# Kernel optimization log

Hardware: AMD Instinct MI355X
Metric: run time of the kernel (lower is better)

Reference implementation:

```python
import jax, jax.numpy as jnp
import numpy as np

N, IN_F, OUT_F, H = 8192, 256, 64, 4
NEG_SLOPE = 0.2


def setup_inputs() -> dict:
    key = jax.random.key(0)
    ks = jax.random.split(key, 8)
    inputs = jax.random.normal(ks[0], (N, IN_F), dtype=jnp.float32)
    # sparse-ish binary adjacency with self loops (sparse.softmax only sees nonzeros)
    adj = (jax.random.uniform(ks[1], (N, N)) < 0.05).astype(jnp.float32)
    idx = jnp.arange(N)
    adj = adj.at[idx, idx].set(1.0)
    stdv = 1.0 / np.sqrt(H * OUT_F)
    weight = jax.random.uniform(ks[2], (IN_F, H * OUT_F), minval=-stdv, maxval=stdv, dtype=jnp.float32)
    bias = jax.random.uniform(ks[3], (1, H * OUT_F), minval=-stdv, maxval=stdv, dtype=jnp.float32)
    # weight_u/v: stdv = 1/sqrt(size(-1)=1) = 1
    weight_u = jax.random.uniform(ks[4], (H, OUT_F, 1), minval=-1.0, maxval=1.0, dtype=jnp.float32)
    weight_v = jax.random.uniform(ks[5], (H, OUT_F, 1), minval=-1.0, maxval=1.0, dtype=jnp.float32)
    stdp = 1.0 / np.sqrt(IN_F)
    proj_w = jax.random.uniform(ks[6], (H * OUT_F, IN_F), minval=-stdp, maxval=stdp, dtype=jnp.float32)
    proj_b = jax.random.uniform(ks[7], (H * OUT_F,), minval=-stdp, maxval=stdp, dtype=jnp.float32)
    return {"inputs": inputs, "adj_mat": adj, "weight": weight, "weight_u": weight_u,
            "weight_v": weight_v, "bias": bias, "proj_w": proj_w, "proj_b": proj_b}


def reference(inputs, adj_mat, weight, weight_u, weight_v, bias, proj_w, proj_b):
    n = inputs.shape[0]
    support = (inputs @ weight).reshape(n, H, OUT_F).transpose(1, 0, 2)  # [H,N,O]
    f1 = jnp.einsum('hno,ho->hn', support, weight_u[..., 0])  # [H,N]
    f2 = jnp.einsum('hno,ho->hn', support, weight_v[..., 0])  # [H,N]
    logits = f1[:, None, :] + f2[:, :, None]                  # [H,N,N]
    w = jax.nn.leaky_relu(logits, NEG_SLOPE)
    masked = w * adj_mat                                      # adj broadcast over heads
    mask = adj_mat != 0.0
    # sparse.softmax over dim 2: softmax restricted to nonzero (edge) positions
    neg = jnp.where(mask, masked, -jnp.inf)
    m = jnp.max(neg, axis=2, keepdims=True)
    m = jnp.where(jnp.isfinite(m), m, 0.0)
    e = jnp.where(mask, jnp.exp(neg - m), 0.0)
    denom = jnp.sum(e, axis=2, keepdims=True)
    attn = e / jnp.where(denom > 0, denom, 1.0)               # [H,N,N]
    out = jnp.einsum('hnm,hmo->hno', attn, support)           # [H,N,O]
    out = out.transpose(1, 0, 2).reshape(n, H * OUT_F)
    out = out + bias
    out = out + inputs @ proj_w.T + proj_b
    return out
```

## Files before the change

kernel.cpp:

```cpp
#include <hip/hip_runtime.h>
#include <hip/hip_bf16.h>

#define N_NODES 8192
#define IN_FEAT 256
#define OUT_F   64
#define NHEAD   4
#define HF      256
#define NEG     0.2f

typedef unsigned short u16;
typedef unsigned long long u64;
typedef __attribute__((ext_vector_type(8))) short short8;
typedef __attribute__((ext_vector_type(4))) float f32x4;

__device__ __forceinline__ u16 f2bf(float f) {
    union { unsigned int u; float f; } v; v.f = f;
    unsigned int r = v.u + 0x7FFFu + ((v.u >> 16) & 1u);
    return (u16)(r >> 16);
}

__global__ __launch_bounds__(256) void k_tr(const float* __restrict__ PW,
                                            float* __restrict__ PWT) {
    __shared__ float t[64][65];
    const int bx = (blockIdx.x & 3) * 64;
    const int by = (blockIdx.x >> 2) * 64;
    const int tx = threadIdx.x & 63;
    const int ty = threadIdx.x >> 6;
    #pragma unroll
    for (int r = ty; r < 64; r += 4)
        t[r][tx] = PW[(size_t)(by + r) * IN_FEAT + bx + tx];
    __syncthreads();
    #pragma unroll
    for (int r = ty; r < 64; r += 4)
        PWT[(size_t)(bx + r) * HF + by + tx] = t[tx][r];
}

#define RPB 4
__global__ __launch_bounds__(256, 8) void k_gemm(
    const float* __restrict__ inp,
    const float* __restrict__ W,
    const float* __restrict__ U,
    const float* __restrict__ V,
    const float* __restrict__ Bias,
    const float* __restrict__ PWT,
    const float* __restrict__ PB,
    const float* __restrict__ adj,
    u16*   __restrict__ suppB,
    float* __restrict__ f1,
    float* __restrict__ f2,
    float* __restrict__ outp,
    u16*   __restrict__ gb,
    float* __restrict__ anum,
    float* __restrict__ aden)
{
    __shared__ __align__(16) float in_lds[RPB][IN_FEAT];
    const int c  = threadIdx.x;
    const int n0 = blockIdx.x * RPB;

    #pragma unroll
    for (int r = 0; r < RPB; ++r)
        in_lds[r][c] = inp[(size_t)(n0 + r) * IN_FEAT + c];
    __syncthreads();

    float accs[RPB], accp[RPB];
    #pragma unroll
    for (int r = 0; r < RPB; ++r) { accs[r] = 0.f; accp[r] = 0.f; }

    const float* wc = W   + c;
    const float* pc = PWT + c;
    float w0 = wc[0 * HF], w1 = wc[1 * HF], w2 = wc[2 * HF], w3 = wc[3 * HF];
    float p0 = pc[0 * HF], p1 = pc[1 * HF], p2 = pc[2 * HF], p3 = pc[3 * HF];

    #pragma unroll 1
    for (int k = 0; k < IN_FEAT; k += 4) {
        const int kn = (k + 4) & 255;
        const float nw0 = wc[(kn + 0) * HF];
        const float nw1 = wc[(kn + 1) * HF];
        const float nw2 = wc[(kn + 2) * HF];
        const float nw3 = wc[(kn + 3) * HF];
        const float np0 = pc[(kn + 0) * HF];
        const float np1 = pc[(kn + 1) * HF];
        const float np2 = pc[(kn + 2) * HF];
        const float np3 = pc[(kn + 3) * HF];
        #pragma unroll
        for (int r = 0; r < RPB; ++r) {
            const float4 xv = *(const float4*)&in_lds[r][k];
            accs[r] = fmaf(xv.x, w0, accs[r]);
            accs[r] = fmaf(xv.y, w1, accs[r]);
            accs[r] = fmaf(xv.z, w2, accs[r]);
            accs[r] = fmaf(xv.w, w3, accs[r]);
            accp[r] = fmaf(xv.x, p0, accp[r]);
            accp[r] = fmaf(xv.y, p1, accp[r]);
            accp[r] = fmaf(xv.z, p2, accp[r]);
            accp[r] = fmaf(xv.w, p3, accp[r]);
        }
        w0 = nw0; w1 = nw1; w2 = nw2; w3 = nw3;
        p0 = np0; p1 = np1; p2 = np2; p3 = np3;
    }

    const int h = c >> 6, lane = c & 63;
    const float uv = U[c], vv = V[c];
    const float bb = Bias[c] + PB[c];

    {
        const int o   = c & 63;
        const int t   = o >> 4;
        const int cc  = o & 15;
        const int jbg = n0 >> 5;
        const int q   = (n0 & 31) >> 3;
        const int el  = n0 & 7;
        union { short s[4]; u64 q8; } sv;
        #pragma unroll
        for (int r = 0; r < RPB; ++r) sv.s[r] = (short)f2bf(accs[r]);
        const size_t word = ((size_t)(h * 256 + jbg) * 4 + t) * 64 + (q << 4) + cc;
        *(u64*)(suppB + word * 8 + el) = sv.q8;
    }

    #pragma unroll
    for (int r = 0; r < RPB; ++r) {
        float s1 = accs[r] * uv, s2 = accs[r] * vv;
        #pragma unroll
        for (int mm = 32; mm > 0; mm >>= 1) {
            s1 += __shfl_xor(s1, mm);
            s2 += __shfl_xor(s2, mm);
        }
        if (lane == 0) {
            f1[h * N_NODES + n0 + r] = s1;
            f2[h * N_NODES + n0 + r] = s2;
        }
        outp[(size_t)(n0 + r) * HF + c] = accp[r] + bb;
    }

    #pragma unroll
    for (int r = 0; r < RPB; ++r)
        anum[(size_t)(n0 + r) * HF + c] = 0.f;
    if (c < 16)
        aden[(size_t)(c >> 2) * N_NODES + n0 + (c & 3)] = 0.f;

    #pragma unroll
    for (int r = 0; r < RPB; ++r) {
        const float* ar = adj + (size_t)(n0 + r) * N_NODES;
        u16* gr = gb + (size_t)(n0 + r) * 1024;
        #pragma unroll
        for (int pass = 0; pass < 4; ++pass) {
            const int w = pass * 256 + c;
            const float4 a0 = *(const float4*)(ar + w * 8);
            const float4 a1 = *(const float4*)(ar + w * 8 + 4);
            gr[w] = (u16)(
                (unsigned)(a0.x != 0.f)        | ((unsigned)(a0.y != 0.f) << 1) |
                ((unsigned)(a0.z != 0.f) << 2) | ((unsigned)(a0.w != 0.f) << 3) |
                ((unsigned)(a1.x != 0.f) << 8) | ((unsigned)(a1.y != 0.f) << 9) |
                ((unsigned)(a1.z != 0.f) << 10)| ((unsigned)(a1.w != 0.f) << 11));
        }
    }
}

__global__ __launch_bounds__(256) void k_prep(const float* __restrict__ f1,
                                              float* __restrict__ f1max,
                                              float* __restrict__ EAB) {
    __shared__ float red[256];
    const int h = blockIdx.x;
    float m = -1e30f;
    for (int j = threadIdx.x; j < N_NODES; j += 256)
        m = fmaxf(m, f1[h * N_NODES + j]);
    red[threadIdx.x] = m;
    __syncthreads();
    for (int s = 128; s > 0; s >>= 1) {
        if (threadIdx.x < s) red[threadIdx.x] = fmaxf(red[threadIdx.x], red[threadIdx.x + s]);
        __syncthreads();
    }
    const float fm = red[0];
    if (threadIdx.x == 0) f1max[h] = fm;
    for (int j = threadIdx.x; j < N_NODES; j += 256) {
        const float d = f1[h * N_NODES + j] - fm;
        EAB[(size_t)h * 2 * N_NODES + 2 * j]     = __expf(d);
        EAB[(size_t)h * 2 * N_NODES + 2 * j + 1] = __expf(NEG * d);
    }
}

#define TI 64
#define NSUB 4
#define JSPLIT_G 4
#define JW (N_NODES / JSPLIT_G)
#define ABW 260

__global__ __launch_bounds__(256, 2) void k_attn_mfma(
    const u16* __restrict__ gbits,
    const u16* __restrict__ suppB,
    const float* __restrict__ EAB,
    const float* __restrict__ f2,
    const float* __restrict__ f1max,
    float* __restrict__ anum,
    float* __restrict__ aden)
{
    __shared__ u16 abits[TI][ABW];

    const int itile = blockIdx.x >> 2;
    const int jwin  = blockIdx.x & 3;
    const int i0    = itile * TI;
    const int J0    = jwin * JW;
    const int wv    = threadIdx.x >> 6;
    const int lane  = threadIdx.x & 63;
    const int col   = lane & 15;
    const int quad  = lane >> 4;

    #pragma unroll
    for (int rr = 0; rr < 16; ++rr) {
        const int r = wv * 16 + rr;
        *(u64*)&abits[r][lane * 4] =
            *(const u64*)(gbits + (size_t)(i0 + r) * 1024 + (J0 >> 3) + lane * 4);
    }
    __syncthreads();

    const int h = wv;
    const float fm = f1max[h];
    float CA[NSUB], CB[NSUB], ls[NSUB];
    #pragma unroll
    for (int s = 0; s < NSUB; ++s) {
        const float f2i = f2[(size_t)h * N_NODES + i0 + s * 16 + col];
        const float g  = fm + f2i;
        const float mi = fmaxf(g, NEG * g);
        CA[s] = __expf(g - mi);
        CB[s] = __expf(NEG * g - mi);
        ls[s] = 0.f;
    }

    const float* EABh = EAB + (size_t)h * 2 * N_NODES + 2 * J0;
    const u16*   sb   = suppB + (size_t)h * 524288
                      + (size_t)(J0 >> 5) * 2048 + lane * 8;

    f32x4 acc[NSUB][4];
    #pragma unroll
    for (int s = 0; s < NSUB; ++s)
        #pragma unroll
        for (int t = 0; t < 4; ++t)
            acc[s][t] = (f32x4){0.f, 0.f, 0.f, 0.f};

    const int qo = quad << 3;

    #pragma unroll 1
    for (int jb = 0; jb < JW; jb += 32) {
        const int jl = jb + qo;
        const u16* fp = sb + (size_t)(jb >> 5) * 2048;
        const short8 bv0 = *(const short8*)(fp);
        const short8 bv1 = *(const short8*)(fp + 512);
        const short8 bv2 = *(const short8*)(fp + 1024);
        const short8 bv3 = *(const short8*)(fp + 1536);
        const float4 ep0 = *(const float4*)(EABh + 2 * jl);
        const float4 ep1 = *(const float4*)(EABh + 2 * jl + 4);
        const float4 ep2 = *(const float4*)(EABh + 2 * jl + 8);
        const float4 ep3 = *(const float4*)(EABh + 2 * jl + 12);
        const int wo = (jb >> 3) + quad;
        u16 gw[NSUB];
        #pragma unroll
        for (int s = 0; s < NSUB; ++s) gw[s] = abits[col + s * 16][wo];

        const float4 ep[4] = {ep0, ep1, ep2, ep3};

        #pragma unroll
        for (int s = 0; s < NSUB; ++s) {
            union { short8 v; unsigned w[4]; } af;
            #pragma unroll
            for (int p = 0; p < 4; ++p) {
                const int je = 2 * p, jo = 2 * p + 1;
                const int she = (je & 3) + ((je >> 2) << 3);
                const int sho = (jo & 3) + ((jo >> 2) << 3);
                float xe = fmaxf(ep[p].x * CA[s], ep[p].y * CB[s]);
                float xo = fmaxf(ep[p].z * CA[s], ep[p].w * CB[s]);
                const unsigned me = 0u - ((unsigned)(gw[s] >> she) & 1u);
                const unsigned mo = 0u - ((unsigned)(gw[s] >> sho) & 1u);
                xe = __uint_as_float(__float_as_uint(xe) & me);
                xo = __uint_as_float(__float_as_uint(xo) & mo);
                ls[s] += xe;
                ls[s] += xo;
                asm("v_cvt_pk_bf16_f32 %0, %1, %2"
                    : "=v"(af.w[p]) : "v"(xe), "v"(xo));
            }
            acc[s][0] = __builtin_amdgcn_mfma_f32_16x16x32_bf16(af.v, bv0, acc[s][0], 0, 0, 0);
            acc[s][1] = __builtin_amdgcn_mfma_f32_16x16x32_bf16(af.v, bv1, acc[s][1], 0, 0, 0);
            acc[s][2] = __builtin_amdgcn_mfma_f32_16x16x32_bf16(af.v, bv2, acc[s][2], 0, 0, 0);
            acc[s][3] = __builtin_amdgcn_mfma_f32_16x16x32_bf16(af.v, bv3, acc[s][3], 0, 0, 0);
        }
    }

    #pragma unroll
    for (int s = 0; s < NSUB; ++s) {
        ls[s] += __shfl_xor(ls[s], 16);
        ls[s] += __shfl_xor(ls[s], 32);
    }
    if (quad == 0) {
        #pragma unroll
        for (int s = 0; s < NSUB; ++s)
            unsafeAtomicAdd(aden + (size_t)h * N_NODES + i0 + s * 16 + col, ls[s]);
    }

    #pragma unroll
    for (int s = 0; s < NSUB; ++s) {
        #pragma unroll
        for (int reg = 0; reg < 4; ++reg) {
            const int irow = (quad << 2) + reg;
            float* ap = anum + (size_t)(i0 + s * 16 + irow) * HF + (h << 6) + col;
            #pragma unroll
            for (int t = 0; t < 4; ++t)
                unsafeAtomicAdd(ap + (t << 4), acc[s][t][reg]);
        }
    }
}

__global__ __launch_bounds__(256) void k_fin(const float* __restrict__ anum,
                                             const float* __restrict__ aden,
                                             float* __restrict__ out) {
    const int c = threadIdx.x;
    const int h = c >> 6;
    #pragma unroll
    for (int rr = 0; rr < 4; ++rr) {
        const int n = blockIdx.x * 4 + rr;
        out[(size_t)n * HF + c] += anum[(size_t)n * HF + c]
                                 / aden[(size_t)h * N_NODES + n];
    }
}

extern "C" void kernel_launch(void* const* d_in, const int* in_sizes, int n_in,
                              void* d_out, int out_size, void* d_ws, size_t ws_size,
                              hipStream_t stream) {
    const float* inp  = (const float*)d_in[0];
    const float* adj  = (const float*)d_in[1];
    const float* W    = (const float*)d_in[2];
    const float* U    = (const float*)d_in[3];
    const float* V    = (const float*)d_in[4];
    const float* Bias = (const float*)d_in[5];
    const float* PW   = (const float*)d_in[6];
    const float* PB   = (const float*)d_in[7];
    float* out = (float*)d_out;

    char* ws = (char*)d_ws;
    u16*   suppB = (u16*)(ws);
    float* f1    = (float*)(ws + (4u << 20));
    float* f2    = (float*)(ws + (4u << 20) + (128u << 10));
    float* f1mx  = (float*)(ws + (4u << 20) + (256u << 10));
    float* PWT   = (float*)(ws + (4u << 20) + (320u << 10));
    float* EAB   = (float*)(ws + (4u << 20) + (576u << 10));
    float* aden  = (float*)(ws + (4u << 20) + (832u << 10));
    u16*   gbits = (u16*)(ws + (8u << 20));
    float* anum  = (float*)(ws + (24u << 20));

    k_tr<<<16, 256, 0, stream>>>(PW, PWT);
    k_gemm<<<N_NODES / RPB, 256, 0, stream>>>(inp, W, U, V, Bias, PWT, PB, adj,
                                              suppB, f1, f2, out, gbits, anum, aden);
    k_prep<<<NHEAD, 256, 0, stream>>>(f1, f1mx, EAB);
    k_attn_mfma<<<(N_NODES / TI) * JSPLIT_G, 256, 0, stream>>>(
        gbits, suppB, EAB, f2, f1mx, anum, aden);
    k_fin<<<N_NODES / 4, 256, 0, stream>>>(anum, aden, out);
}
```

Baseline: 531.1 us.

## Switch attention path to fp16 packed math with LDS-staged exponent tables

Support values and the per-node exponent tables move from bf16/fp32 to fp16. The attention weight computation uses packed half2 multiply, max and mask, with fdot2 for the row sums and fp16 MFMA. The EA/EB tables are staged per block in LDS, and the adjacency bitmask is repacked into contiguous 32-bit words read as bytes. Occupancy is raised to 3 blocks per SIMD and the loop is unrolled by 2. This cuts VALU work and global traffic in the hot loop, at the cost of fp16 range and precision for the exp values and the support values.

```diff
diff --git a/kernel.cpp b/kernel.cpp
--- a/kernel.cpp
+++ b/kernel.cpp
@@ -9,15 +9,11 @@
 #define NEG     0.2f
 
 typedef unsigned short u16;
+typedef unsigned char  u8;
 typedef unsigned long long u64;
-typedef __attribute__((ext_vector_type(8))) short short8;
+typedef _Float16 h2    __attribute__((ext_vector_type(2)));
+typedef _Float16 half8 __attribute__((ext_vector_type(8)));
 typedef __attribute__((ext_vector_type(4))) float f32x4;
-
-__device__ __forceinline__ u16 f2bf(float f) {
-    union { unsigned int u; float f; } v; v.f = f;
-    unsigned int r = v.u + 0x7FFFu + ((v.u >> 16) & 1u);
-    return (u16)(r >> 16);
-}
 
 __global__ __launch_bounds__(256) void k_tr(const float* __restrict__ PW,
                                             float* __restrict__ PWT) {
@@ -45,11 +41,11 @@
     const float* __restrict__ PWT,
     const float* __restrict__ PB,
     const float* __restrict__ adj,
-    u16*   __restrict__ suppB,
+    _Float16* __restrict__ suppB,
     float* __restrict__ f1,
     float* __restrict__ f2,
     float* __restrict__ outp,
-    u16*   __restrict__ gb,
+    unsigned* __restrict__ gb32,
     float* __restrict__ anum,
     float* __restrict__ aden)
 {
@@ -109,9 +105,9 @@
         const int jbg = n0 >> 5;
         const int q   = (n0 & 31) >> 3;
         const int el  = n0 & 7;
-        union { short s[4]; u64 q8; } sv;
-        #pragma unroll
-        for (int r = 0; r < RPB; ++r) sv.s[r] = (short)f2bf(accs[r]);
+        union { _Float16 hh[4]; u64 q8; } sv;
+        #pragma unroll
+        for (int r = 0; r < RPB; ++r) sv.hh[r] = (_Float16)accs[r];
         const size_t word = ((size_t)(h * 256 + jbg) * 4 + t) * 64 + (q << 4) + cc;
         *(u64*)(suppB + word * 8 + el) = sv.q8;
     }
@@ -140,24 +136,27 @@
     #pragma unroll
     for (int r = 0; r < RPB; ++r) {
         const float* ar = adj + (size_t)(n0 + r) * N_NODES;
-        u16* gr = gb + (size_t)(n0 + r) * 1024;
-        #pragma unroll
-        for (int pass = 0; pass < 4; ++pass) {
-            const int w = pass * 256 + c;
-            const float4 a0 = *(const float4*)(ar + w * 8);
-            const float4 a1 = *(const float4*)(ar + w * 8 + 4);
-            gr[w] = (u16)(
+        unsigned wrd = 0;
+        #pragma unroll
+        for (int p = 0; p < 4; ++p) {
+            const int j = c * 32 + p * 8;
+            const float4 a0 = *(const float4*)(ar + j);
+            const float4 a1 = *(const float4*)(ar + j + 4);
+            const unsigned b =
                 (unsigned)(a0.x != 0.f)        | ((unsigned)(a0.y != 0.f) << 1) |
                 ((unsigned)(a0.z != 0.f) << 2) | ((unsigned)(a0.w != 0.f) << 3) |
-                ((unsigned)(a1.x != 0.f) << 8) | ((unsigned)(a1.y != 0.f) << 9) |
-                ((unsigned)(a1.z != 0.f) << 10)| ((unsigned)(a1.w != 0.f) << 11));
-        }
+                ((unsigned)(a1.x != 0.f) << 4) | ((unsigned)(a1.y != 0.f) << 5) |
+                ((unsigned)(a1.z != 0.f) << 6) | ((unsigned)(a1.w != 0.f) << 7);
+            wrd |= b << (8 * p);
+        }
+        gb32[(size_t)(n0 + r) * 256 + c] = wrd;
     }
 }
 
 __global__ __launch_bounds__(256) void k_prep(const float* __restrict__ f1,
                                               float* __restrict__ f1max,
-                                              float* __restrict__ EAB) {
+                                              _Float16* __restrict__ EA16,
+                                              _Float16* __restrict__ EB16) {
     __shared__ float red[256];
     const int h = blockIdx.x;
     float m = -1e30f;
@@ -173,8 +172,8 @@
     if (threadIdx.x == 0) f1max[h] = fm;
     for (int j = threadIdx.x; j < N_NODES; j += 256) {
         const float d = f1[h * N_NODES + j] - fm;
-        EAB[(size_t)h * 2 * N_NODES + 2 * j]     = __expf(d);
-        EAB[(size_t)h * 2 * N_NODES + 2 * j + 1] = __expf(NEG * d);
+        EA16[(size_t)h * N_NODES + j] = (_Float16)__expf(d);
+        EB16[(size_t)h * N_NODES + j] = (_Float16)__expf(NEG * d);
     }
 }
 
@@ -182,18 +181,20 @@
 #define NSUB 4
 #define JSPLIT_G 4
 #define JW (N_NODES / JSPLIT_G)
-#define ABW 260
-
-__global__ __launch_bounds__(256, 2) void k_attn_mfma(
-    const u16* __restrict__ gbits,
-    const u16* __restrict__ suppB,
-    const float* __restrict__ EAB,
+
+__global__ __launch_bounds__(256, 3) void k_attn_mfma(
+    const unsigned* __restrict__ gb32,
+    const _Float16* __restrict__ suppB,
+    const _Float16* __restrict__ EA16,
+    const _Float16* __restrict__ EB16,
     const float* __restrict__ f2,
     const float* __restrict__ f1max,
     float* __restrict__ anum,
     float* __restrict__ aden)
 {
-    __shared__ u16 abits[TI][ABW];
+    __shared__ __align__(16) _Float16 ea_lds[NHEAD][JW];
+    __shared__ __align__(16) _Float16 eb_lds[NHEAD][JW];
+    __shared__ __align__(4)  u8 abyte[TI][260];
 
     const int itile = blockIdx.x >> 2;
     const int jwin  = blockIdx.x & 3;
@@ -204,30 +205,43 @@
     const int col   = lane & 15;
     const int quad  = lane >> 4;
 
+    {
+        const _Float16* gea = EA16 + (size_t)wv * N_NODES + J0;
+        const _Float16* geb = EB16 + (size_t)wv * N_NODES + J0;
+        #pragma unroll
+        for (int it = 0; it < 4; ++it) {
+            const int off = it * 512 + lane * 8;
+            *(float4*)&ea_lds[wv][off] = *(const float4*)(gea + off);
+            *(float4*)&eb_lds[wv][off] = *(const float4*)(geb + off);
+        }
+    }
     #pragma unroll
     for (int rr = 0; rr < 16; ++rr) {
-        const int r = wv * 16 + rr;
-        *(u64*)&abits[r][lane * 4] =
-            *(const u64*)(gbits + (size_t)(i0 + r) * 1024 + (J0 >> 3) + lane * 4);
+        const int r = (wv << 4) + rr;
+        *(unsigned*)&abyte[r][lane * 4] =
+            gb32[(size_t)(i0 + r) * 256 + (J0 >> 5) + lane];
     }
     __syncthreads();
 
     const int h = wv;
     const float fm = f1max[h];
-    float CA[NSUB], CB[NSUB], ls[NSUB];
+    h2 caH[NSUB], cbH[NSUB];
+    float ls[NSUB];
     #pragma unroll
     for (int s = 0; s < NSUB; ++s) {
         const float f2i = f2[(size_t)h * N_NODES + i0 + s * 16 + col];
         const float g  = fm + f2i;
         const float mi = fmaxf(g, NEG * g);
-        CA[s] = __expf(g - mi);
-        CB[s] = __expf(NEG * g - mi);
+        const _Float16 ca = (_Float16)__expf(g - mi);
+        const _Float16 cb = (_Float16)__expf(NEG * g - mi);
+        caH[s][0] = ca; caH[s][1] = ca;
+        cbH[s][0] = cb; cbH[s][1] = cb;
         ls[s] = 0.f;
     }
-
-    const float* EABh = EAB + (size_t)h * 2 * N_NODES + 2 * J0;
-    const u16*   sb   = suppB + (size_t)h * 524288
-                      + (size_t)(J0 >> 5) * 2048 + lane * 8;
+    const h2 ones = {(_Float16)1.0f, (_Float16)1.0f};
+
+    const _Float16* sb = suppB + (size_t)h * 524288
+                       + (size_t)(J0 >> 5) * 2048 + lane * 8;
 
     f32x4 acc[NSUB][4];
     #pragma unroll
@@ -238,48 +252,41 @@
 
     const int qo = quad << 3;
 
-    #pragma unroll 1
+    #pragma unroll 2
     for (int jb = 0; jb < JW; jb += 32) {
         const int jl = jb + qo;
-        const u16* fp = sb + (size_t)(jb >> 5) * 2048;
-        const short8 bv0 = *(const short8*)(fp);
-        const short8 bv1 = *(const short8*)(fp + 512);
-        const short8 bv2 = *(const short8*)(fp + 1024);
-        const short8 bv3 = *(const short8*)(fp + 1536);
-        const float4 ep0 = *(const float4*)(EABh + 2 * jl);
-        const float4 ep1 = *(const float4*)(EABh + 2 * jl + 4);
-        const float4 ep2 = *(const float4*)(EABh + 2 * jl + 8);
-        const float4 ep3 = *(const float4*)(EABh + 2 * jl + 12);
+        const _Float16* fp = sb + (size_t)(jb >> 5) * 2048;
+        const half8 bv0 = *(const half8*)(fp);
+        const half8 bv1 = *(const half8*)(fp + 512);
+        const half8 bv2 = *(const half8*)(fp + 1024);
+        const half8 bv3 = *(const half8*)(fp + 1536);
+
+        union { half8 v; h2 pr[4]; } ea, eb;
+        ea.v = *(const half8*)&ea_lds[h][jl];
+        eb.v = *(const half8*)&eb_lds[h][jl];
         const int wo = (jb >> 3) + quad;
-        u16 gw[NSUB];
-        #pragma unroll
-        for (int s = 0; s < NSUB; ++s) gw[s] = abits[col + s * 16][wo];
-
-        const float4 ep[4] = {ep0, ep1, ep2, ep3};
 
         #pragma unroll
         for (int s = 0; s < NSUB; ++s) {
-            union { short8 v; unsigned w[4]; } af;
+            const unsigned gw = abyte[col + s * 16][wo];
+            union { half8 v; unsigned w[4]; h2 pr[4]; } af;
             #pragma unroll
             for (int p = 0; p < 4; ++p) {
-                const int je = 2 * p, jo = 2 * p + 1;
-                const int she = (je & 3) + ((je >> 2) << 3);
-                const int sho = (jo & 3) + ((jo >> 2) << 3);
-                float xe = fmaxf(ep[p].x * CA[s], ep[p].y * CB[s]);
-                float xo = fmaxf(ep[p].z * CA[s], ep[p].w * CB[s]);
-                const unsigned me = 0u - ((unsigned)(gw[s] >> she) & 1u);
-                const unsigned mo = 0u - ((unsigned)(gw[s] >> sho) & 1u);
-                xe = __uint_as_float(__float_as_uint(xe) & me);
-                xo = __uint_as_float(__float_as_uint(xo) & mo);
-                ls[s] += xe;
-                ls[s] += xo;
-                asm("v_cvt_pk_bf16_f32 %0, %1, %2"
-                    : "=v"(af.w[p]) : "v"(xe), "v"(xo));
+                const h2 pa = ea.pr[p] * caH[s];
+                const h2 pb = eb.pr[p] * cbH[s];
+                const h2 x  = __builtin_elementwise_max(pa, pb);
+                const unsigned mlo = (unsigned)((int)(gw << (31 - 2 * p)) >> 31) & 0x0000FFFFu;
+                const unsigned mhi = (unsigned)((int)(gw << (30 - 2 * p)) >> 31) & 0xFFFF0000u;
+                union { h2 hh; unsigned u; } xu;
+                xu.hh = x;
+                xu.u &= (mlo | mhi);
+                af.w[p] = xu.u;
+                ls[s] = __builtin_amdgcn_fdot2(xu.hh, ones, ls[s], false);
             }
-            acc[s][0] = __builtin_amdgcn_mfma_f32_16x16x32_bf16(af.v, bv0, acc[s][0], 0, 0, 0);
-            acc[s][1] = __builtin_amdgcn_mfma_f32_16x16x32_bf16(af.v, bv1, acc[s][1], 0, 0, 0);
-            acc[s][2] = __builtin_amdgcn_mfma_f32_16x16x32_bf16(af.v, bv2, acc[s][2], 0, 0, 0);
-            acc[s][3] = __builtin_amdgcn_mfma_f32_16x16x32_bf16(af.v, bv3, acc[s][3], 0, 0, 0);
+            acc[s][0] = __builtin_amdgcn_mfma_f32_16x16x32_f16(af.v, bv0, acc[s][0], 0, 0, 0);
+            acc[s][1] = __builtin_amdgcn_mfma_f32_16x16x32_f16(af.v, bv1, acc[s][1], 0, 0, 0);
+            acc[s][2] = __builtin_amdgcn_mfma_f32_16x16x32_f16(af.v, bv2, acc[s][2], 0, 0, 0);
+            acc[s][3] = __builtin_amdgcn_mfma_f32_16x16x32_f16(af.v, bv3, acc[s][3], 0, 0, 0);
         }
     }
 
@@ -334,21 +341,22 @@
     float* out = (float*)d_out;
 
     char* ws = (char*)d_ws;
-    u16*   suppB = (u16*)(ws);
+    _Float16* suppB = (_Float16*)(ws);
     float* f1    = (float*)(ws + (4u << 20));
     float* f2    = (float*)(ws + (4u << 20) + (128u << 10));
     float* f1mx  = (float*)(ws + (4u << 20) + (256u << 10));
     float* PWT   = (float*)(ws + (4u << 20) + (320u << 10));
-    float* EAB   = (float*)(ws + (4u << 20) + (576u << 10));
+    _Float16* EA16 = (_Float16*)(ws + (4u << 20) + (576u << 10));
+    _Float16* EB16 = (_Float16*)(ws + (4u << 20) + (704u << 10));
     float* aden  = (float*)(ws + (4u << 20) + (832u << 10));
-    u16*   gbits = (u16*)(ws + (8u << 20));
+    unsigned* gb32 = (unsigned*)(ws + (8u << 20));
     float* anum  = (float*)(ws + (24u << 20));
 
     k_tr<<<16, 256, 0, stream>>>(PW, PWT);
     k_gemm<<<N_NODES / RPB, 256, 0, stream>>>(inp, W, U, V, Bias, PWT, PB, adj,
-                                              suppB, f1, f2, out, gbits, anum, aden);
-    k_prep<<<NHEAD, 256, 0, stream>>>(f1, f1mx, EAB);
+                                              suppB, f1, f2, out, gb32, anum, aden);
+    k_prep<<<NHEAD, 256, 0, stream>>>(f1, f1mx, EA16, EB16);
     k_attn_mfma<<<(N_NODES / TI) * JSPLIT_G, 256, 0, stream>>>(
-        gbits, suppB, EAB, f2, f1mx, anum, aden);
+        gb32, suppB, EA16, EB16, f2, f1mx, anum, aden);
     k_fin<<<N_NODES / 4, 256, 0, stream>>>(anum, aden, out);
 }
```

Result: faster. 517.3 us (-2.6%).
